# Kernel tuning notes

Hardware: AMD Instinct MI355X
Metric: run time of the kernel (lower is better)

## Reference

```python
import jax, jax.numpy as jnp
from jax import lax
import numpy as np

KSIZE = 3
NUM_GAB = 16
NUM_IMAP = 16
BATCH = 4096


def gabor_bank(theta, sigma, gamma, lambd, psi, ksize=KSIZE):
    # vectorized version of the original triple Python loop
    offs = jnp.arange(ksize, dtype=theta.dtype) - 1.0  # (x-1), (y-1) in source
    xg, yg = jnp.meshgrid(offs, offs, indexing='ij')   # [K,K]
    c = jnp.cos(theta)[:, None, None]
    s = jnp.sin(theta)[:, None, None]
    xt = xg * c + yg * s        # [F,K,K]
    yt = -xg * s + yg * c
    sx = sigma[:, None, None]
    sy = (sigma / gamma)[:, None, None]
    env = jnp.exp(-0.5 * (xt ** 2 / sx ** 2 + yt ** 2 / sy ** 2))
    car = jnp.cos(2.0 * jnp.pi * xt / lambd[:, None, None] + psi[:, None, None])
    return env * car  # [F,K,K]


def maxpool2(x):
    return lax.reduce_window(x, -jnp.inf, lax.max, (1, 1, 2, 2), (1, 1, 2, 2), 'VALID')


def setup_inputs() -> dict:
    key = jax.random.key(0)
    ks = jax.random.split(key, 12)
    x = jax.random.normal(ks[0], (BATCH, 1, 28, 28), dtype=jnp.float32)
    theta = jax.random.uniform(ks[1], (NUM_GAB,), minval=0.0, maxval=180.0)
    sigma = jax.random.uniform(ks[2], (NUM_GAB,), minval=0.0, maxval=360.0)
    gamma = jax.random.uniform(ks[3], (NUM_GAB,), minval=0.0, maxval=1.0)
    lambd = jax.random.uniform(ks[4], (NUM_GAB,), minval=2.0, maxval=10.0)
    psi = jnp.zeros((NUM_GAB,), dtype=jnp.float32)
    conv2_w = jax.random.normal(ks[5], (64, 32, 3, 3), dtype=jnp.float32) * 0.05
    conv2_b = jnp.zeros((64,), dtype=jnp.float32)
    fc1_w = jax.random.normal(ks[6], (128, 3136), dtype=jnp.float32) * 0.02
    fc1_b = jnp.zeros((128,), dtype=jnp.float32)
    fc2_w = jax.random.normal(ks[7], (10, 128), dtype=jnp.float32) * 0.1
    fc2_b = jnp.zeros((10,), dtype=jnp.float32)
    return dict(x=x, theta=theta, sigma=sigma, gamma=gamma, lambd=lambd, psi=psi,
                conv2_w=conv2_w, conv2_b=conv2_b, fc1_w=fc1_w, fc1_b=fc1_b,
                fc2_w=fc2_w, fc2_b=fc2_b)


def reference(x, theta, sigma, gamma, lambd, psi, conv2_w, conv2_b, fc1_w, fc1_b, fc2_w, fc2_b):
    kern = gabor_bank(theta, sigma, gamma, lambd, psi)          # [16,3,3]
    imaps = jnp.zeros((NUM_IMAP, KSIZE, KSIZE), dtype=x.dtype).at[:, 1, 1].set(1.0)
    w1 = jnp.concatenate([kern, imaps], axis=0)[:, None]         # [32,1,3,3]
    dn = ('NCHW', 'OIHW', 'NCHW')
    out = lax.conv_general_dilated(x, w1, (1, 1), [(1, 1), (1, 1)], dimension_numbers=dn)
    out = maxpool2(jax.nn.relu(out))                             # [B,32,14,14]
    out = lax.conv_general_dilated(out, conv2_w, (1, 1), [(1, 1), (1, 1)], dimension_numbers=dn)
    out = maxpool2(jax.nn.relu(out + conv2_b[None, :, None, None]))  # [B,64,7,7]
    out = out.reshape(out.shape[0], -1)                          # [B,3136]
    out = jax.nn.relu(out @ fc1_w.T + fc1_b)                     # dropout = identity (eval)
    out = out @ fc2_w.T + fc2_b                                  # [B,10]
    return out
```

## Files before the change

### kernel.cpp

```cpp
#include <hip/hip_runtime.h>
#include <hip/hip_bf16.h>

#define BATCH 4096

typedef unsigned short u16;
typedef _Float16 half2v __attribute__((ext_vector_type(2)));
typedef _Float16 half4 __attribute__((ext_vector_type(4)));
typedef _Float16 half8 __attribute__((ext_vector_type(8)));
typedef short bs8 __attribute__((ext_vector_type(8)));
typedef u16 u16x4 __attribute__((ext_vector_type(4)));
typedef float floatx4 __attribute__((ext_vector_type(4)));
typedef float floatx16 __attribute__((ext_vector_type(16)));

__device__ inline u16 f2bf_hw(float f) {
    __hip_bfloat16 b = __float2bfloat16(f);
    return *(u16*)&b;
}

__global__ __launch_bounds__(256) void prep_kernel(
        const float* __restrict__ theta, const float* __restrict__ sigma,
        const float* __restrict__ gamma, const float* __restrict__ lambd,
        const float* __restrict__ psi, const float* __restrict__ conv2_w,
        const float* __restrict__ fc1_w, _Float16* __restrict__ w1h,
        _Float16* __restrict__ w2h, u16* __restrict__ wbf) {
    int id = blockIdx.x * 256 + threadIdx.x;
    if (id < 512) {
        int g = id >> 4, t = id & 15;
        float v = 0.0f;
        if (t < 9) {
            int i = t / 3, j = t % 3;
            float xg = (float)i - 1.0f;
            float yg = (float)j - 1.0f;
            if (g < 16) {
                float th = theta[g];
                float c = cosf(th), s = sinf(th);
                float xt = xg * c + yg * s;
                float yt = -xg * s + yg * c;
                float sx = sigma[g];
                float sy = sx / gamma[g];
                float env = expf(-0.5f *
                                 (xt * xt / (sx * sx) + yt * yt / (sy * sy)));
                float car =
                    cosf(6.28318530717958647692f * xt / lambd[g] + psi[g]);
                v = env * car;
            } else {
                v = (t == 4) ? 1.0f : 0.0f;
            }
        }
        w1h[id] = (_Float16)v;
    } else if (id < 512 + 18432) {
        int t2 = id - 512;
        int tap = t2 / 2048, rem = t2 % 2048;
        int oc = rem / 32, k = rem % 32;
        int ic = (k >> 1) + 16 * (k & 1);
        w2h[t2] = (_Float16)conv2_w[(oc * 32 + ic) * 9 + tap];
    } else {
        int i4 = id - 18944;
        float4 v = ((const float4*)fc1_w)[i4];
        u16x4 o;
        o[0] = f2bf_hw(v.x);
        o[1] = f2bf_hw(v.y);
        o[2] = f2bf_hw(v.z);
        o[3] = f2bf_hw(v.w);
        ((u16x4*)wbf)[i4] = o;
    }
}

__global__ __launch_bounds__(256) void fused_conv_kernel(
        const float* __restrict__ x, const _Float16* __restrict__ w1h,
        const _Float16* __restrict__ w2h, const float* __restrict__ conv2_b,
        u16* __restrict__ a2) {
    __shared__ _Float16 img16[30][36];
    __shared__ __align__(16) _Float16 a1s[16][16][40];
    __shared__ __align__(16) u16 out2[64 * 49];

    int t = threadIdx.x;
    int n = blockIdx.x;
    int lane = t & 63;
    int w = t >> 6;
    int l16 = lane & 15;
    int quad = lane >> 4;
    int l32 = lane & 31;
    int h = lane >> 5;

    int nt = w & 1;
    int mt0 = w >> 1;
    int oc = nt * 32 + l32;
    half8 bE[9], bO[9];
    const _Float16* bp = w2h + (size_t)oc * 32 + h * 8;
#pragma unroll
    for (int tt = 0; tt < 9; ++tt) {
        bE[tt] = *(const half8*)(bp + tt * 2048);
        bO[tt] = *(const half8*)(bp + tt * 2048 + 16);
    }
    float bias = conv2_b[oc];

    for (int i = t; i < 1280; i += 256)
        ((int4*)&a1s[0][0][0])[i] = int4{0, 0, 0, 0};
    const float* xim = x + (size_t)n * 784;
    for (int i = t; i < 900; i += 256) {
        int r = i / 30, c = i % 30;
        float v = (r >= 1 && r <= 28 && c >= 1 && c <= 28)
                      ? xim[(r - 1) * 28 + (c - 1)]
                      : 0.0f;
        img16[r][c] = (_Float16)v;
    }
    __syncthreads();

    half4 b1a = *(const half4*)&w1h[l16 * 16 + quad * 4];
    half4 b1b = *(const half4*)&w1h[(16 + l16) * 16 + quad * 4];
    int t0 = quad * 4;
    int u0 = t0 < 9 ? t0 : 8, u1 = t0 + 1 < 9 ? t0 + 1 : 8;
    int u2 = t0 + 2 < 9 ? t0 + 2 : 8, u3 = t0 + 3 < 9 ? t0 + 3 : 8;
    int off0 = (u0 / 3) * 36 + (u0 % 3);
    int off1 = (u1 / 3) * 36 + (u1 % 3);
    int off2 = (u2 / 3) * 36 + (u2 % 3);
    int off3 = (u3 / 3) * 36 + (u3 % 3);
    int sy = (l16 & 3) >> 1, sx = l16 & 1;

    int pool0 = w * 4 + (l16 >> 2);
    int a14 = pool0 >= 14 ? 1 : 0;
    int b14 = pool0 - 14 * a14;
    int pl0 = w * 4 + quad;
    int pa = pl0 >= 14 ? 1 : 0;
    int pb = pl0 - 14 * pa;

    for (int mt = w; mt < 49; mt += 4) {
        const _Float16* p = &img16[2 * a14 + sy][2 * b14 + sx];
        half4 av;
        av[0] = p[off0];
        av[1] = p[off1];
        av[2] = p[off2];
        av[3] = p[off3];
        floatx4 c0 = {0.f, 0.f, 0.f, 0.f};
        floatx4 c1 = {0.f, 0.f, 0.f, 0.f};
        c0 = __builtin_amdgcn_mfma_f32_16x16x16f16(av, b1a, c0, 0, 0, 0);
        c1 = __builtin_amdgcn_mfma_f32_16x16x16f16(av, b1b, c1, 0, 0, 0);
        float m0 = fmaxf(fmaxf(c0[0], c0[1]), fmaxf(c0[2], c0[3]));
        float m1 = fmaxf(fmaxf(c1[0], c1[1]), fmaxf(c1[2], c1[3]));
        half2v pk;
        pk[0] = (_Float16)fmaxf(m0, 0.0f);
        pk[1] = (_Float16)fmaxf(m1, 0.0f);
        *(half2v*)&a1s[1 + pa][1 + pb][2 * l16] = pk;
        a14 += 1; b14 += 2;
        if (b14 >= 14) { b14 -= 14; a14 += 1; }
        pa += 1; pb += 2;
        if (pb >= 14) { pb -= 14; pa += 1; }
    }
    __syncthreads();

    for (int mt = mt0; mt < 7; mt += 2) {
        int pool = mt * 8 + (l32 >> 2);
        int sub = l32 & 3;
        int pc = pool < 49 ? pool : 48;
        int y = 2 * (pc / 7) + (sub >> 1);
        int xq = 2 * (pc % 7) + (sub & 1);
        const _Float16* ap = &a1s[y][xq][h * 8];
        floatx16 acc = {};
#pragma unroll
        for (int tt = 0; tt < 9; ++tt) {
            int ao = ((tt / 3) * 16 + (tt % 3)) * 40;
            half8 avE = *(const half8*)(ap + ao);
            half8 avO = *(const half8*)(ap + ao + 16);
            acc = __builtin_amdgcn_mfma_f32_32x32x16_f16(avE, bE[tt], acc,
                                                         0, 0, 0);
            acc = __builtin_amdgcn_mfma_f32_32x32x16_f16(avO, bO[tt], acc,
                                                         0, 0, 0);
        }
#pragma unroll
        for (int rg = 0; rg < 4; ++rg) {
            int pl = mt * 8 + 2 * rg + h;
            if (pl < 49) {
                float v0 = acc[rg * 4 + 0];
                float v1 = acc[rg * 4 + 1];
                float v2 = acc[rg * 4 + 2];
                float v3 = acc[rg * 4 + 3];
                float mx = fmaxf(fmaxf(v0, v1), fmaxf(v2, v3));
                out2[oc * 49 + pl] = f2bf_hw(fmaxf(mx + bias, 0.0f));
            }
        }
    }
    __syncthreads();

    uint2* dst = (uint2*)(a2 + (size_t)n * 3136);
    const uint2* src = (const uint2*)&out2[0];
    for (int i = t; i < 784; i += 256) dst[i] = src[i];
}

__global__ __launch_bounds__(1024) void fc_kernel(
        const u16* __restrict__ A, const u16* __restrict__ Wbf,
        const float* __restrict__ fc1_b, const float* __restrict__ fc2_w,
        const float* __restrict__ fc2_b, float* __restrict__ out) {
    __shared__ float Hs[8][16][132];
    int tid = threadIdx.x;
    int lane = tid & 63;
    int w = tid >> 6;
    int l16 = lane & 15;
    int quad = lane >> 4;
    int kq = w >> 1;
    int nh = w & 1;
    int m0 = blockIdx.x * 16;

    const u16* aptr = A + (size_t)(m0 + l16) * 3136 + quad * 8;
    const u16* b0 = Wbf + (size_t)(nh * 64 + l16) * 3136 + quad * 8;
    const u16* b1 = b0 + 16 * 3136;
    const u16* b2 = b0 + 32 * 3136;
    const u16* b3 = b0 + 48 * 3136;

    floatx4 ac0 = {0.f, 0.f, 0.f, 0.f};
    floatx4 ac1 = {0.f, 0.f, 0.f, 0.f};
    floatx4 ac2 = {0.f, 0.f, 0.f, 0.f};
    floatx4 ac3 = {0.f, 0.f, 0.f, 0.f};
#pragma unroll 4
    for (int s = kq; s < 98; s += 8) {
        int k0 = s * 32;
        bs8 av = *(const bs8*)(aptr + k0);
        bs8 bv0 = *(const bs8*)(b0 + k0);
        bs8 bv1 = *(const bs8*)(b1 + k0);
        bs8 bv2 = *(const bs8*)(b2 + k0);
        bs8 bv3 = *(const bs8*)(b3 + k0);
        ac0 = __builtin_amdgcn_mfma_f32_16x16x32_bf16(av, bv0, ac0, 0, 0, 0);
        ac1 = __builtin_amdgcn_mfma_f32_16x16x32_bf16(av, bv1, ac1, 0, 0, 0);
        ac2 = __builtin_amdgcn_mfma_f32_16x16x32_bf16(av, bv2, ac2, 0, 0, 0);
        ac3 = __builtin_amdgcn_mfma_f32_16x16x32_bf16(av, bv3, ac3, 0, 0, 0);
    }
    int nb = nh * 64 + l16;
#pragma unroll
    for (int r = 0; r < 4; ++r) {
        int mr = quad * 4 + r;
        Hs[kq][mr][nb] = ac0[r];
        Hs[kq][mr][nb + 16] = ac1[r];
        Hs[kq][mr][nb + 32] = ac2[r];
        Hs[kq][mr][nb + 48] = ac3[r];
    }
    __syncthreads();

    for (int i = tid; i < 2048; i += 1024) {
        int m = i >> 7, k = i & 127;
        float s = Hs[0][m][k] + Hs[1][m][k] + Hs[2][m][k] + Hs[3][m][k] +
                  Hs[4][m][k] + Hs[5][m][k] + Hs[6][m][k] + Hs[7][m][k];
        Hs[0][m][k] = s;
    }
    __syncthreads();

    if (tid < 160) {
        int m = tid / 10, j = tid % 10;
        const float* wr = fc2_w + j * 128;
        float acc = fc2_b[j];
#pragma unroll 16
        for (int k = 0; k < 128; ++k)
            acc += fmaxf(Hs[0][m][k] + fc1_b[k], 0.0f) * wr[k];
        out[(size_t)(m0 + m) * 10 + j] = acc;
    }
}

extern "C" void kernel_launch(void* const* d_in, const int* in_sizes, int n_in,
                              void* d_out, int out_size, void* d_ws,
                              size_t ws_size, hipStream_t stream) {
    const float* x       = (const float*)d_in[0];
    const float* theta   = (const float*)d_in[1];
    const float* sigma   = (const float*)d_in[2];
    const float* gamma   = (const float*)d_in[3];
    const float* lambd   = (const float*)d_in[4];
    const float* psi     = (const float*)d_in[5];
    const float* conv2_w = (const float*)d_in[6];
    const float* conv2_b = (const float*)d_in[7];
    const float* fc1_w   = (const float*)d_in[8];
    const float* fc1_b   = (const float*)d_in[9];
    const float* fc2_w   = (const float*)d_in[10];
    const float* fc2_b   = (const float*)d_in[11];
    float* out = (float*)d_out;

    char* ws = (char*)d_ws;
    u16* a2 = (u16*)ws;
    _Float16* w1h = (_Float16*)(ws + 25690112ull);
    _Float16* w2h = (_Float16*)(ws + 25691136ull);
    u16* wbf = (u16*)(ws + 25728000ull);

    prep_kernel<<<466, 256, 0, stream>>>(theta, sigma, gamma, lambd, psi,
                                         conv2_w, fc1_w, w1h, w2h, wbf);
    fused_conv_kernel<<<BATCH, 256, 0, stream>>>(x, w1h, w2h, conv2_b, a2);
    fc_kernel<<<BATCH / 16, 1024, 0, stream>>>(a2, wbf, fc1_b, fc2_w, fc2_b,
                                               out);
}
```

Baseline: 160.4 us.

## Zero only conv1 halo, software-pipeline im2col loads, halve FC rows per block

```diff
diff --git a/kernel.cpp b/kernel.cpp
--- a/kernel.cpp
+++ b/kernel.cpp
@@ -95,14 +95,20 @@
     }
     float bias = conv2_b[oc];
 
-    for (int i = t; i < 1280; i += 256)
-        ((int4*)&a1s[0][0][0])[i] = int4{0, 0, 0, 0};
+    for (int i = t; i < 240; i += 256) {
+        int pos = i >> 2, ch = i & 3;
+        int r, c;
+        if (pos < 16)      { r = 0;        c = pos; }
+        else if (pos < 32) { r = 15;       c = pos - 16; }
+        else if (pos < 46) { r = pos - 31; c = 0; }
+        else               { r = pos - 45; c = 15; }
+        *(int4*)&a1s[r][c][ch * 8] = int4{0, 0, 0, 0};
+    }
     const float* xim = x + (size_t)n * 784;
-    for (int i = t; i < 900; i += 256) {
-        int r = i / 30, c = i % 30;
-        float v = (r >= 1 && r <= 28 && c >= 1 && c <= 28)
-                      ? xim[(r - 1) * 28 + (c - 1)]
-                      : 0.0f;
+    for (int i = t; i < 960; i += 256) {
+        int r = i >> 5, c = i & 31;
+        bool inter = (r >= 1) & (r <= 28) & (c >= 1) & (c <= 28);
+        float v = inter ? xim[(r - 1) * 28 + (c - 1)] : 0.0f;
         img16[r][c] = (_Float16)v;
     }
     __syncthreads();
@@ -125,27 +131,37 @@
     int pa = pl0 >= 14 ? 1 : 0;
     int pb = pl0 - 14 * pa;
 
+    const _Float16* p0 = &img16[2 * a14 + sy][2 * b14 + sx];
+    half4 avc;
+    avc[0] = p0[off0];
+    avc[1] = p0[off1];
+    avc[2] = p0[off2];
+    avc[3] = p0[off3];
+
     for (int mt = w; mt < 49; mt += 4) {
-        const _Float16* p = &img16[2 * a14 + sy][2 * b14 + sx];
-        half4 av;
-        av[0] = p[off0];
-        av[1] = p[off1];
-        av[2] = p[off2];
-        av[3] = p[off3];
+        a14 += 1; b14 += 2;
+        if (b14 >= 14) { b14 -= 14; a14 += 1; }
+        half4 avn;
+        if (mt + 4 < 49) {
+            const _Float16* p = &img16[2 * a14 + sy][2 * b14 + sx];
+            avn[0] = p[off0];
+            avn[1] = p[off1];
+            avn[2] = p[off2];
+            avn[3] = p[off3];
+        }
         floatx4 c0 = {0.f, 0.f, 0.f, 0.f};
         floatx4 c1 = {0.f, 0.f, 0.f, 0.f};
-        c0 = __builtin_amdgcn_mfma_f32_16x16x16f16(av, b1a, c0, 0, 0, 0);
-        c1 = __builtin_amdgcn_mfma_f32_16x16x16f16(av, b1b, c1, 0, 0, 0);
+        c0 = __builtin_amdgcn_mfma_f32_16x16x16f16(avc, b1a, c0, 0, 0, 0);
+        c1 = __builtin_amdgcn_mfma_f32_16x16x16f16(avc, b1b, c1, 0, 0, 0);
         float m0 = fmaxf(fmaxf(c0[0], c0[1]), fmaxf(c0[2], c0[3]));
         float m1 = fmaxf(fmaxf(c1[0], c1[1]), fmaxf(c1[2], c1[3]));
         half2v pk;
         pk[0] = (_Float16)fmaxf(m0, 0.0f);
         pk[1] = (_Float16)fmaxf(m1, 0.0f);
         *(half2v*)&a1s[1 + pa][1 + pb][2 * l16] = pk;
-        a14 += 1; b14 += 2;
-        if (b14 >= 14) { b14 -= 14; a14 += 1; }
         pa += 1; pb += 2;
         if (pb >= 14) { pb -= 14; pa += 1; }
+        avc = avn;
     }
     __syncthreads();
 
@@ -191,7 +207,7 @@
         const u16* __restrict__ A, const u16* __restrict__ Wbf,
         const float* __restrict__ fc1_b, const float* __restrict__ fc2_w,
         const float* __restrict__ fc2_b, float* __restrict__ out) {
-    __shared__ float Hs[8][16][132];
+    __shared__ float Hs[8][8][132];
     int tid = threadIdx.x;
     int lane = tid & 63;
     int w = tid >> 6;
@@ -199,9 +215,9 @@
     int quad = lane >> 4;
     int kq = w >> 1;
     int nh = w & 1;
-    int m0 = blockIdx.x * 16;
-
-    const u16* aptr = A + (size_t)(m0 + l16) * 3136 + quad * 8;
+    int m0 = blockIdx.x * 8;
+
+    const u16* aptr = A + (size_t)(m0 + (l16 & 7)) * 3136 + quad * 8;
     const u16* b0 = Wbf + (size_t)(nh * 64 + l16) * 3136 + quad * 8;
     const u16* b1 = b0 + 16 * 3136;
     const u16* b2 = b0 + 32 * 3136;
@@ -225,17 +241,19 @@
         ac3 = __builtin_amdgcn_mfma_f32_16x16x32_bf16(av, bv3, ac3, 0, 0, 0);
     }
     int nb = nh * 64 + l16;
+    if (quad < 2) {
 #pragma unroll
-    for (int r = 0; r < 4; ++r) {
-        int mr = quad * 4 + r;
-        Hs[kq][mr][nb] = ac0[r];
-        Hs[kq][mr][nb + 16] = ac1[r];
-        Hs[kq][mr][nb + 32] = ac2[r];
-        Hs[kq][mr][nb + 48] = ac3[r];
-    }
-    __syncthreads();
-
-    for (int i = tid; i < 2048; i += 1024) {
+        for (int r = 0; r < 4; ++r) {
+            int mr = quad * 4 + r;
+            Hs[kq][mr][nb] = ac0[r];
+            Hs[kq][mr][nb + 16] = ac1[r];
+            Hs[kq][mr][nb + 32] = ac2[r];
+            Hs[kq][mr][nb + 48] = ac3[r];
+        }
+    }
+    __syncthreads();
+
+    for (int i = tid; i < 1024; i += 1024) {
         int m = i >> 7, k = i & 127;
         float s = Hs[0][m][k] + Hs[1][m][k] + Hs[2][m][k] + Hs[3][m][k] +
                   Hs[4][m][k] + Hs[5][m][k] + Hs[6][m][k] + Hs[7][m][k];
@@ -243,7 +261,7 @@
     }
     __syncthreads();
 
-    if (tid < 160) {
+    if (tid < 80) {
         int m = tid / 10, j = tid % 10;
         const float* wr = fc2_w + j * 128;
         float acc = fc2_b[j];
@@ -280,6 +298,6 @@
     prep_kernel<<<466, 256, 0, stream>>>(theta, sigma, gamma, lambd, psi,
                                          conv2_w, fc1_w, w1h, w2h, wbf);
     fused_conv_kernel<<<BATCH, 256, 0, stream>>>(x, w1h, w2h, conv2_b, a2);
-    fc_kernel<<<BATCH / 16, 1024, 0, stream>>>(a2, wbf, fc1_b, fc2_w, fc2_b,
-                                               out);
-}
+    fc_kernel<<<BATCH / 8, 1024, 0, stream>>>(a2, wbf, fc1_b, fc2_w, fc2_b,
+                                              out);
+}
```

New measurement: 187.2 us. +16.7%, slower.
